# Kernel tuning notes

Hardware: AMD Instinct MI355X
Metric: run time of the kernel (lower is better)

## Reference

```python
import jax, jax.numpy as jnp
import numpy as np

OUT_F, IN_F = 4096, 4096
WEIGHT_NUMEL = OUT_F * IN_F
NUM_CHUNKS, CHUNK_SIZE = 16384, 1024
D_ALPHA, HIDDEN = 64, 256
TOKENS = 256


def setup_inputs() -> dict:
    key = jax.random.key(0)
    ks = jax.random.split(key, 7)
    s = 0.05  # keep activations in a sane range
    return {
        "x": jax.random.normal(ks[0], (TOKENS, IN_F), jnp.float32),
        "codebook": jax.random.normal(ks[1], (NUM_CHUNKS, D_ALPHA), jnp.float32) * s,
        "w1": jax.random.normal(ks[2], (HIDDEN, D_ALPHA), jnp.float32) * s,
        "b1": jax.random.normal(ks[3], (HIDDEN,), jnp.float32) * s,
        "w2": jax.random.normal(ks[4], (CHUNK_SIZE, HIDDEN), jnp.float32) * s,
        "b2": jax.random.normal(ks[5], (CHUNK_SIZE,), jnp.float32) * s,
        "bias": jax.random.normal(ks[6], (OUT_F,), jnp.float32) * s,
    }


def reference(x, codebook, w1, b1, w2, b2, bias):
    # materialize_weight: alpha = codebook[start:start+num_chunks] (here: all rows)
    alpha = codebook[:NUM_CHUNKS]                                  # [num_chunks, d_alpha]
    # shared decoder psi: Linear -> GELU(exact) -> Linear (chunked loop == single GEMM)
    h = jax.nn.gelu(alpha @ w1.T + b1, approximate=False)          # [num_chunks, hidden]
    chunks = h @ w2.T + b2                                         # [num_chunks, chunk_size]
    w = chunks.reshape(-1)[:WEIGHT_NUMEL].reshape(OUT_F, IN_F)     # assemble weight
    # F.linear(x, w, b) = x @ w.T + b
    return x @ w.T + bias
```

## Files before the change

### kernel.cpp

```cpp
#include <hip/hip_runtime.h>
#include <math.h>

#define OUT_F      4096
#define IN_F       4096
#define NUM_CHUNKS 16384
#define CHUNK_SIZE 1024
#define D_ALPHA    64
#define HIDDEN     256
#define TOKENS     256
#define ZY         4

typedef __attribute__((ext_vector_type(8))) __bf16 bf16x8;
typedef __attribute__((ext_vector_type(4))) __bf16 bf16x4;
typedef __attribute__((ext_vector_type(4))) float f32x4;

__device__ __forceinline__ void gl2lds16(const void* g, void* l) {
    __builtin_amdgcn_global_load_lds(
        (const __attribute__((address_space(1))) void*)g,
        (__attribute__((address_space(3))) void*)l,
        16, 0, 0);
}

__global__ __launch_bounds__(256) void prep_kernel(
    const float* __restrict__ cb, const float* __restrict__ w1,
    const float* __restrict__ b1, const float* __restrict__ x,
    const float* __restrict__ b2, const float* __restrict__ w2,
    __bf16* __restrict__ H, __bf16* __restrict__ xb,
    float* __restrict__ xb2, __bf16* __restrict__ w2t) {
    __shared__ char smem[32 * 64 * 4];
    const int b   = blockIdx.x;
    const int tid = threadIdx.x;

    if (b < 512) {
        float* sa = (float*)smem;
        const int c0 = b * 32;
        {
            const float4* cb4 = reinterpret_cast<const float4*>(cb) + (size_t)b * 512;
            float4* sa4 = reinterpret_cast<float4*>(sa);
            sa4[tid]       = cb4[tid];
            sa4[tid + 256] = cb4[tid + 256];
        }
        __syncthreads();
        float4 w[16];
        const float4* w1r = reinterpret_cast<const float4*>(w1 + tid * 64);
#pragma unroll
        for (int q = 0; q < 16; ++q) w[q] = w1r[q];
        const float bias1 = b1[tid];
        for (int c = 0; c < 32; ++c) {
            float acc = bias1;
            const float4* sav = reinterpret_cast<const float4*>(sa + c * 64);
#pragma unroll
            for (int q = 0; q < 16; ++q) {
                float4 a4 = sav[q];
                acc += a4.x * w[q].x + a4.y * w[q].y + a4.z * w[q].z + a4.w * w[q].w;
            }
            float g = 0.5f * acc * (1.0f + erff(acc * 0.70710678118654752f));
            H[(size_t)(c0 + c) * 256 + tid] = (__bf16)g;
        }
    } else if (b < 768) {
        float* ws_ = (float*)smem;
        const int t = b - 512;
        const float4* xr  = reinterpret_cast<const float4*>(x + (size_t)t * IN_F);
        const float4* b24 = reinterpret_cast<const float4*>(b2);
        bf16x4* xb4 = reinterpret_cast<bf16x4*>(xb + (size_t)t * IN_F);
        float acc = 0.0f;
#pragma unroll
        for (int ii = 0; ii < 4; ++ii) {
            const int idx = ii * 256 + tid;
            float4 v = xr[idx];
            bf16x4 o;
            o.x = (__bf16)v.x; o.y = (__bf16)v.y; o.z = (__bf16)v.z; o.w = (__bf16)v.w;
            xb4[idx] = o;
            float4 bb = b24[idx & 255];
            acc += v.x * bb.x + v.y * bb.y + v.z * bb.z + v.w * bb.w;
        }
#pragma unroll
        for (int off = 32; off > 0; off >>= 1) acc += __shfl_down(acc, off, 64);
        if ((tid & 63) == 0) ws_[tid >> 6] = acc;
        __syncthreads();
        if (tid == 0) xb2[t] = ws_[0] + ws_[1] + ws_[2] + ws_[3];
    } else {
        float (*tile)[33] = (float (*)[33])smem;
        const int bb = b - 768;
        const int h0 = (bb & 7) * 32;
        const int p0 = (bb >> 3) * 32;
        const int r = tid >> 5;
        const int c = tid & 31;
#pragma unroll
        for (int ii = 0; ii < 4; ++ii)
            tile[r + 8 * ii][c] = w2[(size_t)(p0 + r + 8 * ii) * HIDDEN + h0 + c];
        __syncthreads();
#pragma unroll
        for (int ii = 0; ii < 4; ++ii)
            w2t[(size_t)(h0 + r + 8 * ii) * CHUNK_SIZE + p0 + c] =
                (__bf16)tile[c][r + 8 * ii];
    }
}

template <int EPI>
__global__ __launch_bounds__(256) void gemm_bt_mfma64(
    const __bf16* __restrict__ A, const __bf16* __restrict__ B,
    const float* __restrict__ bias, const float* __restrict__ rowterm,
    float* __restrict__ C, int M, int N, int K, int k_per_split) {
    constexpr int BK = 64;
    __shared__ __bf16 sA[64 * BK];
    __shared__ __bf16 sB[64 * BK];

    const int tid = threadIdx.x;
    const int m0 = blockIdx.y * 64;
    const int n0 = blockIdx.x * 64;
    const int kz0 = blockIdx.z * k_per_split;
    const int kz1 = kz0 + k_per_split;

    const int srow = tid >> 3;
    const int scol = (tid & 7) * 8;
    const __bf16* gA0 = A + (size_t)(m0 + srow) * K + scol;
    const __bf16* gA1 = A + (size_t)(m0 + srow + 32) * K + scol;
    const __bf16* gB0 = B + (size_t)(n0 + srow) * K + scol;
    const __bf16* gB1 = B + (size_t)(n0 + srow + 32) * K + scol;
    __bf16* lA0 = sA + tid * 8;
    __bf16* lA1 = sA + tid * 8 + 2048;
    __bf16* lB0 = sB + tid * 8;
    __bf16* lB1 = sB + tid * 8 + 2048;

    const int wave = tid >> 6;
    const int lane = tid & 63;
    const int wm = (wave & 1) * 32;
    const int wn = (wave >> 1) * 32;
    const int fr = lane & 15;
    const int fq = lane >> 4;

    f32x4 acc[2][2] = {};

    for (int k0 = kz0; k0 < kz1; k0 += BK) {
        gl2lds16(gA0 + k0, lA0);
        gl2lds16(gA1 + k0, lA1);
        gl2lds16(gB0 + k0, lB0);
        gl2lds16(gB1 + k0, lB1);
        __syncthreads();

        bf16x8 af[2][2], bfr[2][2];
#pragma unroll
        for (int i = 0; i < 2; ++i)
#pragma unroll
            for (int u = 0; u < 2; ++u) {
                const int ak = u * 32 + fq * 8;
                af[i][u]  = *reinterpret_cast<const bf16x8*>(
                    sA + (wm + i * 16 + fr) * BK + ak);
                bfr[i][u] = *reinterpret_cast<const bf16x8*>(
                    sB + (wn + i * 16 + fr) * BK + ak);
            }
#pragma unroll
        for (int i = 0; i < 2; ++i)
#pragma unroll
            for (int j = 0; j < 2; ++j) {
                acc[i][j] = __builtin_amdgcn_mfma_f32_16x16x32_bf16(
                    af[i][0], bfr[j][0], acc[i][j], 0, 0, 0);
                acc[i][j] = __builtin_amdgcn_mfma_f32_16x16x32_bf16(
                    af[i][1], bfr[j][1], acc[i][j], 0, 0, 0);
            }
        __syncthreads();
    }

    const size_t zoff = (EPI == 0) ? (size_t)blockIdx.z * (size_t)M * N : 0;
#pragma unroll
    for (int j = 0; j < 2; ++j) {
        const int col = n0 + wn + j * 16 + fr;
        const float bv = (EPI == 1) ? bias[col] : 0.0f;
#pragma unroll
        for (int i = 0; i < 2; ++i) {
            const int rbase = m0 + wm + i * 16 + fq * 4;
#pragma unroll
            for (int r = 0; r < 4; ++r) {
                float v = acc[i][j][r] + bv;
                if (EPI == 1) v += rowterm[rbase + r];
                C[zoff + (size_t)(rbase + r) * N + col] = v;
            }
        }
    }
}

__global__ __launch_bounds__(256) void reduce_y(
    const float* __restrict__ part, __bf16* __restrict__ Y) {
    const int i = blockIdx.x * blockDim.x + threadIdx.x;
    const int n4 = 1024 * HIDDEN / 4;
    if (i >= n4) return;
    float4 s = {0, 0, 0, 0};
#pragma unroll
    for (int z = 0; z < ZY; ++z) {
        float4 p = reinterpret_cast<const float4*>(part + (size_t)z * 1024 * HIDDEN)[i];
        s.x += p.x; s.y += p.y; s.z += p.z; s.w += p.w;
    }
    bf16x4 o;
    o.x = (__bf16)s.x; o.y = (__bf16)s.y; o.z = (__bf16)s.z; o.w = (__bf16)s.w;
    reinterpret_cast<bf16x4*>(Y)[i] = o;
}

extern "C" void kernel_launch(void* const* d_in, const int* in_sizes, int n_in,
                              void* d_out, int out_size, void* d_ws, size_t ws_size,
                              hipStream_t stream) {
    const float* x        = (const float*)d_in[0];
    const float* codebook = (const float*)d_in[1];
    const float* w1       = (const float*)d_in[2];
    const float* b1       = (const float*)d_in[3];
    const float* w2       = (const float*)d_in[4];
    const float* b2       = (const float*)d_in[5];
    const float* bias     = (const float*)d_in[6];
    float* out = (float*)d_out;

    char* ws = (char*)d_ws;
    __bf16* xb  = (__bf16*)(ws);
    __bf16* w2t = (__bf16*)(ws + (2u << 20));
    __bf16* H   = (__bf16*)(ws + (3u << 20));
    __bf16* Y   = (__bf16*)(ws + (11u << 20));
    float*  xb2 = (float*)(ws + (12u << 20));
    float*  Yp  = (float*)(ws + (13u << 20));

    prep_kernel<<<1024, 256, 0, stream>>>(codebook, w1, b1, x, b2, w2,
                                          H, xb, xb2, w2t);

    {
        dim3 grid(HIDDEN / 64, 1024 / 64, ZY);
        gemm_bt_mfma64<0><<<grid, 256, 0, stream>>>(
            xb, w2t, nullptr, nullptr, Yp, 1024, HIDDEN, 1024, 1024 / ZY);
    }

    reduce_y<<<(1024 * HIDDEN / 4) / 256, 256, 0, stream>>>(Yp, Y);

    {
        dim3 grid(OUT_F / 64, TOKENS / 64, 1);
        gemm_bt_mfma64<1><<<grid, 256, 0, stream>>>(
            Y, H, bias, xb2, out, TOKENS, OUT_F, 1024, 1024);
    }
}
```

Baseline: 114.4 us.

## Use MFMA for codebook hidden layer, drop split-K reduction, widen BK

The codebook-to-hidden layer (alpha @ w1.T + GELU) now converts both operands to bf16 in LDS and computes 64x64 tiles with MFMA, replacing the scalar fp32 FMA loop. The Y GEMM no longer splits K four ways, so the separate reduce kernel and the fp32 partial buffer go away, and the GEMM writes bf16 directly. Both GEMMs use a 128-wide K tile to halve the number of barrier iterations. In exchange, the first layer now runs in bf16 instead of fp32, which lowers its precision, and the Y GEMM launches far fewer blocks (64), which may leave compute units idle.

```diff
diff --git a/kernel.cpp b/kernel.cpp
--- a/kernel.cpp
+++ b/kernel.cpp
@@ -8,7 +8,6 @@
 #define D_ALPHA    64
 #define HIDDEN     256
 #define TOKENS     256
-#define ZY         4
 
 typedef __attribute__((ext_vector_type(8))) __bf16 bf16x8;
 typedef __attribute__((ext_vector_type(4))) __bf16 bf16x4;
@@ -27,39 +26,70 @@
     const float* __restrict__ b2, const float* __restrict__ w2,
     __bf16* __restrict__ H, __bf16* __restrict__ xb,
     float* __restrict__ xb2, __bf16* __restrict__ w2t) {
-    __shared__ char smem[32 * 64 * 4];
+    __shared__ char smem[16384];
     const int b   = blockIdx.x;
     const int tid = threadIdx.x;
 
-    if (b < 512) {
-        float* sa = (float*)smem;
-        const int c0 = b * 32;
-        {
-            const float4* cb4 = reinterpret_cast<const float4*>(cb) + (size_t)b * 512;
-            float4* sa4 = reinterpret_cast<float4*>(sa);
-            sa4[tid]       = cb4[tid];
-            sa4[tid + 256] = cb4[tid + 256];
-        }
-        __syncthreads();
-        float4 w[16];
-        const float4* w1r = reinterpret_cast<const float4*>(w1 + tid * 64);
-#pragma unroll
-        for (int q = 0; q < 16; ++q) w[q] = w1r[q];
-        const float bias1 = b1[tid];
-        for (int c = 0; c < 32; ++c) {
-            float acc = bias1;
-            const float4* sav = reinterpret_cast<const float4*>(sa + c * 64);
-#pragma unroll
-            for (int q = 0; q < 16; ++q) {
-                float4 a4 = sav[q];
-                acc += a4.x * w[q].x + a4.y * w[q].y + a4.z * w[q].z + a4.w * w[q].w;
-            }
-            float g = 0.5f * acc * (1.0f + erff(acc * 0.70710678118654752f));
-            H[(size_t)(c0 + c) * 256 + tid] = (__bf16)g;
-        }
-    } else if (b < 768) {
+    if (b < 1024) {
+        const int by = b >> 2;
+        const int bx = b & 3;
+        const int c0 = by * 64, h0 = bx * 64;
+        __bf16* sA = (__bf16*)smem;
+        __bf16* sB = (__bf16*)(smem + 8192);
+        const float4* cb4 = reinterpret_cast<const float4*>(cb) + (size_t)by * 1024;
+        const float4* w14 = reinterpret_cast<const float4*>(w1) + (size_t)bx * 1024;
+#pragma unroll
+        for (int q = 0; q < 4; ++q) {
+            const int idx = q * 256 + tid;
+            float4 va = cb4[idx];
+            float4 vb = w14[idx];
+            bf16x4 oa, ob;
+            oa.x = (__bf16)va.x; oa.y = (__bf16)va.y; oa.z = (__bf16)va.z; oa.w = (__bf16)va.w;
+            ob.x = (__bf16)vb.x; ob.y = (__bf16)vb.y; ob.z = (__bf16)vb.z; ob.w = (__bf16)vb.w;
+            *reinterpret_cast<bf16x4*>(sA + idx * 4) = oa;
+            *reinterpret_cast<bf16x4*>(sB + idx * 4) = ob;
+        }
+        __syncthreads();
+        const int wave = tid >> 6, lane = tid & 63;
+        const int wm = (wave & 1) * 32, wn = (wave >> 1) * 32;
+        const int fr = lane & 15, fq = lane >> 4;
+        f32x4 acc[2][2] = {};
+        bf16x8 af[2][2], bv[2][2];
+#pragma unroll
+        for (int i = 0; i < 2; ++i)
+#pragma unroll
+            for (int u = 0; u < 2; ++u) {
+                af[i][u] = *reinterpret_cast<const bf16x8*>(
+                    sA + (wm + i * 16 + fr) * 64 + u * 32 + fq * 8);
+                bv[i][u] = *reinterpret_cast<const bf16x8*>(
+                    sB + (wn + i * 16 + fr) * 64 + u * 32 + fq * 8);
+            }
+#pragma unroll
+        for (int u = 0; u < 2; ++u)
+#pragma unroll
+            for (int i = 0; i < 2; ++i)
+#pragma unroll
+                for (int j = 0; j < 2; ++j)
+                    acc[i][j] = __builtin_amdgcn_mfma_f32_16x16x32_bf16(
+                        af[i][u], bv[j][u], acc[i][j], 0, 0, 0);
+#pragma unroll
+        for (int j = 0; j < 2; ++j) {
+            const int col = h0 + wn + j * 16 + fr;
+            const float bb = b1[col];
+#pragma unroll
+            for (int i = 0; i < 2; ++i) {
+                const int rbase = c0 + wm + i * 16 + fq * 4;
+#pragma unroll
+                for (int r = 0; r < 4; ++r) {
+                    float v = acc[i][j][r] + bb;
+                    float g = 0.5f * v * (1.0f + erff(v * 0.70710678118654752f));
+                    H[(size_t)(rbase + r) * 256 + col] = (__bf16)g;
+                }
+            }
+        }
+    } else if (b < 1280) {
         float* ws_ = (float*)smem;
-        const int t = b - 512;
+        const int t = b - 1024;
         const float4* xr  = reinterpret_cast<const float4*>(x + (size_t)t * IN_F);
         const float4* b24 = reinterpret_cast<const float4*>(b2);
         bf16x4* xb4 = reinterpret_cast<bf16x4*>(xb + (size_t)t * IN_F);
@@ -81,7 +111,7 @@
         if (tid == 0) xb2[t] = ws_[0] + ws_[1] + ws_[2] + ws_[3];
     } else {
         float (*tile)[33] = (float (*)[33])smem;
-        const int bb = b - 768;
+        const int bb = b - 1280;
         const int h0 = (bb & 7) * 32;
         const int p0 = (bb >> 3) * 32;
         const int r = tid >> 5;
@@ -97,103 +127,91 @@
     }
 }
 
-template <int EPI>
-__global__ __launch_bounds__(256) void gemm_bt_mfma64(
+template <int BK, int EPI>
+__global__ __launch_bounds__(256) void gemm_bt64(
     const __bf16* __restrict__ A, const __bf16* __restrict__ B,
     const float* __restrict__ bias, const float* __restrict__ rowterm,
-    float* __restrict__ C, int M, int N, int K, int k_per_split) {
-    constexpr int BK = 64;
+    void* __restrict__ Cv, int M, int N, int K) {
     __shared__ __bf16 sA[64 * BK];
     __shared__ __bf16 sB[64 * BK];
-
     const int tid = threadIdx.x;
     const int m0 = blockIdx.y * 64;
     const int n0 = blockIdx.x * 64;
-    const int kz0 = blockIdx.z * k_per_split;
-    const int kz1 = kz0 + k_per_split;
-
-    const int srow = tid >> 3;
-    const int scol = (tid & 7) * 8;
-    const __bf16* gA0 = A + (size_t)(m0 + srow) * K + scol;
-    const __bf16* gA1 = A + (size_t)(m0 + srow + 32) * K + scol;
-    const __bf16* gB0 = B + (size_t)(n0 + srow) * K + scol;
-    const __bf16* gB1 = B + (size_t)(n0 + srow + 32) * K + scol;
-    __bf16* lA0 = sA + tid * 8;
-    __bf16* lA1 = sA + tid * 8 + 2048;
-    __bf16* lB0 = sB + tid * 8;
-    __bf16* lB1 = sB + tid * 8 + 2048;
-
-    const int wave = tid >> 6;
-    const int lane = tid & 63;
-    const int wm = (wave & 1) * 32;
-    const int wn = (wave >> 1) * 32;
-    const int fr = lane & 15;
-    const int fq = lane >> 4;
+
+    constexpr int NC = BK / 32;
+    int rowc[NC], colc[NC];
+#pragma unroll
+    for (int c = 0; c < NC; ++c) {
+        const int flat = c * 2048 + tid * 8;
+        rowc[c] = flat / BK;
+        colc[c] = flat % BK;
+    }
+
+    const int wave = tid >> 6, lane = tid & 63;
+    const int wm = (wave & 1) * 32, wn = (wave >> 1) * 32;
+    const int fr = lane & 15, fq = lane >> 4;
 
     f32x4 acc[2][2] = {};
 
-    for (int k0 = kz0; k0 < kz1; k0 += BK) {
-        gl2lds16(gA0 + k0, lA0);
-        gl2lds16(gA1 + k0, lA1);
-        gl2lds16(gB0 + k0, lB0);
-        gl2lds16(gB1 + k0, lB1);
-        __syncthreads();
-
-        bf16x8 af[2][2], bfr[2][2];
-#pragma unroll
-        for (int i = 0; i < 2; ++i)
-#pragma unroll
-            for (int u = 0; u < 2; ++u) {
-                const int ak = u * 32 + fq * 8;
-                af[i][u]  = *reinterpret_cast<const bf16x8*>(
-                    sA + (wm + i * 16 + fr) * BK + ak);
-                bfr[i][u] = *reinterpret_cast<const bf16x8*>(
-                    sB + (wn + i * 16 + fr) * BK + ak);
-            }
-#pragma unroll
-        for (int i = 0; i < 2; ++i)
-#pragma unroll
-            for (int j = 0; j < 2; ++j) {
-                acc[i][j] = __builtin_amdgcn_mfma_f32_16x16x32_bf16(
-                    af[i][0], bfr[j][0], acc[i][j], 0, 0, 0);
-                acc[i][j] = __builtin_amdgcn_mfma_f32_16x16x32_bf16(
-                    af[i][1], bfr[j][1], acc[i][j], 0, 0, 0);
-            }
-        __syncthreads();
-    }
-
-    const size_t zoff = (EPI == 0) ? (size_t)blockIdx.z * (size_t)M * N : 0;
-#pragma unroll
-    for (int j = 0; j < 2; ++j) {
-        const int col = n0 + wn + j * 16 + fr;
-        const float bv = (EPI == 1) ? bias[col] : 0.0f;
-#pragma unroll
-        for (int i = 0; i < 2; ++i) {
-            const int rbase = m0 + wm + i * 16 + fq * 4;
-#pragma unroll
-            for (int r = 0; r < 4; ++r) {
-                float v = acc[i][j][r] + bv;
-                if (EPI == 1) v += rowterm[rbase + r];
-                C[zoff + (size_t)(rbase + r) * N + col] = v;
-            }
-        }
-    }
-}
-
-__global__ __launch_bounds__(256) void reduce_y(
-    const float* __restrict__ part, __bf16* __restrict__ Y) {
-    const int i = blockIdx.x * blockDim.x + threadIdx.x;
-    const int n4 = 1024 * HIDDEN / 4;
-    if (i >= n4) return;
-    float4 s = {0, 0, 0, 0};
-#pragma unroll
-    for (int z = 0; z < ZY; ++z) {
-        float4 p = reinterpret_cast<const float4*>(part + (size_t)z * 1024 * HIDDEN)[i];
-        s.x += p.x; s.y += p.y; s.z += p.z; s.w += p.w;
-    }
-    bf16x4 o;
-    o.x = (__bf16)s.x; o.y = (__bf16)s.y; o.z = (__bf16)s.z; o.w = (__bf16)s.w;
-    reinterpret_cast<bf16x4*>(Y)[i] = o;
+    for (int k0 = 0; k0 < K; k0 += BK) {
+#pragma unroll
+        for (int c = 0; c < NC; ++c) {
+            gl2lds16(A + (size_t)(m0 + rowc[c]) * K + k0 + colc[c],
+                     sA + c * 2048 + tid * 8);
+            gl2lds16(B + (size_t)(n0 + rowc[c]) * K + k0 + colc[c],
+                     sB + c * 2048 + tid * 8);
+        }
+        __syncthreads();
+
+#pragma unroll
+        for (int u = 0; u < BK / 32; ++u) {
+            bf16x8 af[2], bv[2];
+#pragma unroll
+            for (int i = 0; i < 2; ++i) {
+                af[i] = *reinterpret_cast<const bf16x8*>(
+                    sA + (wm + i * 16 + fr) * BK + u * 32 + fq * 8);
+                bv[i] = *reinterpret_cast<const bf16x8*>(
+                    sB + (wn + i * 16 + fr) * BK + u * 32 + fq * 8);
+            }
+#pragma unroll
+            for (int i = 0; i < 2; ++i)
+#pragma unroll
+                for (int j = 0; j < 2; ++j)
+                    acc[i][j] = __builtin_amdgcn_mfma_f32_16x16x32_bf16(
+                        af[i], bv[j], acc[i][j], 0, 0, 0);
+        }
+        __syncthreads();
+    }
+
+    if (EPI == 0) {
+        __bf16* C = (__bf16*)Cv;
+#pragma unroll
+        for (int j = 0; j < 2; ++j) {
+            const int col = n0 + wn + j * 16 + fr;
+#pragma unroll
+            for (int i = 0; i < 2; ++i) {
+                const int rbase = m0 + wm + i * 16 + fq * 4;
+#pragma unroll
+                for (int r = 0; r < 4; ++r)
+                    C[(size_t)(rbase + r) * N + col] = (__bf16)acc[i][j][r];
+            }
+        }
+    } else {
+        float* C = (float*)Cv;
+#pragma unroll
+        for (int j = 0; j < 2; ++j) {
+            const int col = n0 + wn + j * 16 + fr;
+            const float bvs = bias[col];
+#pragma unroll
+            for (int i = 0; i < 2; ++i) {
+                const int rbase = m0 + wm + i * 16 + fq * 4;
+#pragma unroll
+                for (int r = 0; r < 4; ++r)
+                    C[(size_t)(rbase + r) * N + col] =
+                        acc[i][j][r] + bvs + rowterm[rbase + r];
+            }
+        }
+    }
 }
 
 extern "C" void kernel_launch(void* const* d_in, const int* in_sizes, int n_in,
@@ -214,22 +232,19 @@
     __bf16* H   = (__bf16*)(ws + (3u << 20));
     __bf16* Y   = (__bf16*)(ws + (11u << 20));
     float*  xb2 = (float*)(ws + (12u << 20));
-    float*  Yp  = (float*)(ws + (13u << 20));
-
-    prep_kernel<<<1024, 256, 0, stream>>>(codebook, w1, b1, x, b2, w2,
+
+    prep_kernel<<<1536, 256, 0, stream>>>(codebook, w1, b1, x, b2, w2,
                                           H, xb, xb2, w2t);
 
     {
-        dim3 grid(HIDDEN / 64, 1024 / 64, ZY);
-        gemm_bt_mfma64<0><<<grid, 256, 0, stream>>>(
-            xb, w2t, nullptr, nullptr, Yp, 1024, HIDDEN, 1024, 1024 / ZY);
-    }
-
-    reduce_y<<<(1024 * HIDDEN / 4) / 256, 256, 0, stream>>>(Yp, Y);
+        dim3 grid(HIDDEN / 64, 1024 / 64, 1);
+        gemm_bt64<128, 0><<<grid, 256, 0, stream>>>(
+            xb, w2t, nullptr, nullptr, Y, 1024, HIDDEN, 1024);
+    }
 
     {
         dim3 grid(OUT_F / 64, TOKENS / 64, 1);
-        gemm_bt_mfma64<1><<<grid, 256, 0, stream>>>(
-            Y, H, bias, xb2, out, TOKENS, OUT_F, 1024, 1024);
-    }
-}
+        gemm_bt64<128, 1><<<grid, 256, 0, stream>>>(
+            Y, H, bias, xb2, out, TOKENS, OUT_F, 1024);
+    }
+}
```

Measured after the change: 105.9 us, median of 2. -7.4%, faster.
